# Kernel optimization log

Hardware: AMD Instinct MI355X
Metric: run time of the kernel (lower is better)

The kernel has to match this reference:

```python
import jax, jax.numpy as jnp
import numpy as np

N_, C_, D_, H_, W_ = 2, 96, 32, 64, 64
KC, VC, HEADS = 96, 96, 4


def setup_inputs() -> dict:
    key = jax.random.key(0)
    ks = jax.random.split(key, 9)
    s = 0.05
    return {
        "x": jax.random.normal(ks[0], (N_, C_, D_, H_, W_), jnp.float32),
        "Wk": jax.random.normal(ks[1], (KC, C_), jnp.float32) * s,
        "bk": jax.random.normal(ks[2], (KC,), jnp.float32) * s,
        "Wq": jax.random.normal(ks[3], (KC, C_), jnp.float32) * s,
        "bq": jax.random.normal(ks[4], (KC,), jnp.float32) * s,
        "Wv": jax.random.normal(ks[5], (VC, C_), jnp.float32) * s,
        "bv": jax.random.normal(ks[6], (VC,), jnp.float32) * s,
        "Wr": jax.random.normal(ks[7], (C_, VC), jnp.float32) * s,
        "br": jax.random.normal(ks[8], (C_,), jnp.float32) * s,
    }


def reference(x, Wk, bk, Wq, bq, Wv, bv, Wr, br):
    n, c, d, h, w = x.shape
    Nvox = d * h * w
    xf = x.reshape(n, c, Nvox)  # [n, c, N]
    # 1x1x1 convs == channel matmuls
    keys = jnp.einsum('oc,ncN->noN', Wk, xf) + bk[None, :, None]
    queries = jnp.einsum('oc,ncN->noN', Wq, xf) + bq[None, :, None]
    values = jnp.einsum('oc,ncN->noN', Wv, xf) + bv[None, :, None]
    hk = KC // HEADS
    hv = VC // HEADS
    k = keys.reshape(n, HEADS, hk, Nvox)
    q = queries.reshape(n, HEADS, hk, Nvox)
    v = values.reshape(n, HEADS, hv, Nvox)
    # key softmax over sequence (N), query softmax over head channels (hk)
    k = jax.nn.softmax(k, axis=3)
    q = jax.nn.softmax(q, axis=2)
    # context[n,h,k,v] = key @ value^T ; attended = context^T @ query
    context = jnp.einsum('nhkN,nhvN->nhkv', k, v)
    attended = jnp.einsum('nhkv,nhkN->nhvN', context, q)
    agg = attended.reshape(n, VC, Nvox)
    out = jnp.einsum('ov,nvN->noN', Wr, agg) + br[None, :, None]
    return out.reshape(n, c, d, h, w)
```

## Files before the change

kernel.cpp:

```cpp
#include <hip/hip_runtime.h>


#define NV 131072
#define CC 96
#define NB 2
#define HK 24
#define PAD 68
#define BPN 384
#define TILES_N 2048

__global__ __launch_bounds__(256) void k_prep(
    const float* __restrict__ Wq, const float* __restrict__ Wk,
    const float* __restrict__ Wv,
    float* __restrict__ Wqt, float* __restrict__ Wkt, float* __restrict__ Wvt)
{
    const int i = blockIdx.x * 256 + threadIdx.x;
    if (i >= CC * CC) return;
    const int h = i / (HK * CC);
    const int r = i % (HK * CC);
    const int c = r / HK;
    const int j = r % HK;
    const int src = (h * HK + j) * CC + c;
    Wqt[i] = Wq[src];
    Wkt[i] = Wk[src];
    Wvt[i] = Wv[src];
}

__global__ __launch_bounds__(256) void k_fused(
    const float* __restrict__ x,
    const float* __restrict__ Wqt, const float* __restrict__ bq,
    const float* __restrict__ Wkt, const float* __restrict__ bk,
    const float* __restrict__ Wvt, const float* __restrict__ bv,
    float* __restrict__ qsm, float* __restrict__ ctx, float* __restrict__ ksum)
{
    __shared__ float eks[4 * HK * PAD];
    __shared__ float vls[4 * HK * PAD];
    const int tid = threadIdx.x;
    const int pl  = tid & 63;
    const int gu  = __builtin_amdgcn_readfirstlane(tid >> 6);
    const int n   = blockIdx.x / BPN;
    const int r0  = blockIdx.x % BPN;
    const int a   = pl >> 3, b = pl & 7;

    float* __restrict__ ek = eks + gu * HK * PAD;
    float* __restrict__ vl = vls + gu * HK * PAD;
    const float* __restrict__ Wqh = Wqt + gu * HK * CC;
    const float* __restrict__ Wkh = Wkt + gu * HK * CC;
    const float* __restrict__ Wvh = Wvt + gu * HK * CC;

    float cacc[9];
#pragma unroll
    for (int k = 0; k < 9; ++k) cacc[k] = 0.f;
    float ksacc = 0.f;

    for (int tt = r0; tt < TILES_N; tt += BPN) {
        const size_t xb = (size_t)n * CC * NV + (size_t)tt * 64 + pl;

        float aq[HK], ak[HK], av[HK];
#pragma unroll
        for (int j = 0; j < HK; ++j) {
            aq[j] = bq[gu * HK + j];
            ak[j] = bk[gu * HK + j];
            av[j] = bv[gu * HK + j];
        }
        for (int ch = 0; ch < 6; ++ch) {
            float xr[16];
#pragma unroll
            for (int u = 0; u < 16; ++u)
                xr[u] = x[xb + (size_t)(ch * 16 + u) * NV];
#pragma unroll
            for (int u = 0; u < 16; ++u) {
                const float* __restrict__ w = Wqh + (ch * 16 + u) * HK;
#pragma unroll
                for (int j = 0; j < HK; ++j) aq[j] = fmaf(w[j], xr[u], aq[j]);
            }
#pragma unroll
            for (int u = 0; u < 16; ++u) {
                const float* __restrict__ w = Wkh + (ch * 16 + u) * HK;
#pragma unroll
                for (int j = 0; j < HK; ++j) ak[j] = fmaf(w[j], xr[u], ak[j]);
            }
#pragma unroll
            for (int u = 0; u < 16; ++u) {
                const float* __restrict__ w = Wvh + (ch * 16 + u) * HK;
#pragma unroll
                for (int j = 0; j < HK; ++j) av[j] = fmaf(w[j], xr[u], av[j]);
            }
        }

        {
            float mx = aq[0];
#pragma unroll
            for (int j = 1; j < HK; ++j) mx = fmaxf(mx, aq[j]);
            float s = 0.f;
#pragma unroll
            for (int j = 0; j < HK; ++j) { aq[j] = __expf(aq[j] - mx); s += aq[j]; }
            const float inv = 1.f / s;
            float4* __restrict__ qs4 = (float4*)qsm;
            const size_t qb4 = ((size_t)n * 24 + gu * 6) * NV + (size_t)tt * 64 + pl;
#pragma unroll
            for (int jj = 0; jj < 6; ++jj) {
                float4 t;
                t.x = aq[4 * jj + 0] * inv;
                t.y = aq[4 * jj + 1] * inv;
                t.z = aq[4 * jj + 2] * inv;
                t.w = aq[4 * jj + 3] * inv;
                qs4[qb4 + (size_t)jj * NV] = t;
            }
        }

#pragma unroll
        for (int j = 0; j < HK; ++j) ek[j * PAD + pl] = __expf(ak[j]);
#pragma unroll
        for (int j = 0; j < HK; ++j) vl[j * PAD + pl] = av[j];

        if (pl < HK) {
            const float4* __restrict__ rp = (const float4*)(ek + pl * PAD);
            float s = 0.f;
#pragma unroll
            for (int q = 0; q < 16; ++q) {
                const float4 t = rp[q];
                s += t.x + t.y + t.z + t.w;
            }
            ksacc += s;
        }

#pragma unroll
        for (int q = 0; q < 16; ++q) {
            float4 e4[3], v4[3];
#pragma unroll
            for (int i = 0; i < 3; ++i)
                e4[i] = ((const float4*)(ek + (a + 8 * i) * PAD))[q];
#pragma unroll
            for (int j = 0; j < 3; ++j)
                v4[j] = ((const float4*)(vl + (b + 8 * j) * PAD))[q];
#pragma unroll
            for (int i = 0; i < 3; ++i)
#pragma unroll
                for (int j = 0; j < 3; ++j) {
                    float t = cacc[i * 3 + j];
                    t = fmaf(e4[i].x, v4[j].x, t);
                    t = fmaf(e4[i].y, v4[j].y, t);
                    t = fmaf(e4[i].z, v4[j].z, t);
                    t = fmaf(e4[i].w, v4[j].w, t);
                    cacc[i * 3 + j] = t;
                }
        }
    }

#pragma unroll
    for (int i = 0; i < 3; ++i)
#pragma unroll
        for (int j = 0; j < 3; ++j)
            atomicAdd(&ctx[((size_t)n * CC + gu * HK + a + 8 * i) * HK + b + 8 * j],
                      cacc[i * 3 + j]);
    if (pl < HK) atomicAdd(&ksum[n * CC + gu * HK + pl], ksacc);
}

__global__ __launch_bounds__(256) void k_combine(
    const float* __restrict__ Wr, const float* __restrict__ ctx,
    const float* __restrict__ ksum, float* __restrict__ Mnt)
{
    const int n = blockIdx.x;
    for (int i = threadIdx.x; i < CC * CC; i += 256) {
        const int kg = i / CC, o = i % CC, h = kg / HK;
        float a = 0.f;
        for (int v = 0; v < HK; ++v)
            a += Wr[o * CC + h * HK + v] * ctx[((size_t)n * CC + kg) * HK + v];
        Mnt[((size_t)n * CC + kg) * CC + o] = a / ksum[n * CC + kg];
    }
}

__global__ __launch_bounds__(256) void k_out(
    const float* __restrict__ qsm, const float* __restrict__ Mnt,
    const float* __restrict__ br, float* __restrict__ out)
{
    const int tid = threadIdx.x;
    const int pl  = tid & 63;
    const int w   = __builtin_amdgcn_readfirstlane(tid >> 6);
    const int n   = blockIdx.x >> 10;
    const int pt  = blockIdx.x & 1023;
    const size_t p0 = (size_t)pt * 128 + pl;

    const float* __restrict__ Mb = Mnt + ((size_t)n * CC) * CC + w * HK;
    const float4* __restrict__ q4 = (const float4*)qsm + (size_t)n * 24 * NV + p0;

    float a0[HK], a1[HK];
#pragma unroll
    for (int j = 0; j < HK; ++j) { a0[j] = br[w * HK + j]; a1[j] = a0[j]; }

#pragma unroll 2
    for (int qg = 0; qg < 24; ++qg) {
        const float4 v0 = q4[(size_t)qg * NV];
        const float4 v1 = q4[(size_t)qg * NV + 64];
        const float* __restrict__ m0 = Mb + (size_t)(4 * qg + 0) * CC;
        const float* __restrict__ m1 = Mb + (size_t)(4 * qg + 1) * CC;
        const float* __restrict__ m2 = Mb + (size_t)(4 * qg + 2) * CC;
        const float* __restrict__ m3 = Mb + (size_t)(4 * qg + 3) * CC;
#pragma unroll
        for (int j = 0; j < HK; ++j) {
            a0[j] = fmaf(m0[j], v0.x, a0[j]);
            a1[j] = fmaf(m0[j], v1.x, a1[j]);
        }
#pragma unroll
        for (int j = 0; j < HK; ++j) {
            a0[j] = fmaf(m1[j], v0.y, a0[j]);
            a1[j] = fmaf(m1[j], v1.y, a1[j]);
        }
#pragma unroll
        for (int j = 0; j < HK; ++j) {
            a0[j] = fmaf(m2[j], v0.z, a0[j]);
            a1[j] = fmaf(m2[j], v1.z, a1[j]);
        }
#pragma unroll
        for (int j = 0; j < HK; ++j) {
            a0[j] = fmaf(m3[j], v0.w, a0[j]);
            a1[j] = fmaf(m3[j], v1.w, a1[j]);
        }
    }

    float* __restrict__ ob = out + ((size_t)n * CC + (size_t)w * HK) * NV + p0;
#pragma unroll
    for (int j = 0; j < HK; ++j) {
        ob[(size_t)j * NV]      = a0[j];
        ob[(size_t)j * NV + 64] = a1[j];
    }
}

extern "C" void kernel_launch(void* const* d_in, const int* in_sizes, int n_in,
                              void* d_out, int out_size, void* d_ws, size_t ws_size,
                              hipStream_t stream) {
    const float* x  = (const float*)d_in[0];
    const float* Wk = (const float*)d_in[1];
    const float* bk = (const float*)d_in[2];
    const float* Wq = (const float*)d_in[3];
    const float* bq = (const float*)d_in[4];
    const float* Wv = (const float*)d_in[5];
    const float* bv = (const float*)d_in[6];
    const float* Wr = (const float*)d_in[7];
    const float* br = (const float*)d_in[8];
    float* out = (float*)d_out;

    float* ws = (float*)d_ws;
    const size_t BIG = (size_t)NB * CC * NV;
    float* qsm  = ws;
    float* ctx  = ws + BIG;
    float* ksum = ctx + (size_t)NB * CC * HK;
    float* Mnt  = ksum + (size_t)NB * CC;
    float* Wqt  = Mnt + (size_t)NB * CC * CC;
    float* Wkt  = Wqt + CC * CC;
    float* Wvt  = Wkt + CC * CC;

    hipMemsetAsync(ctx, 0, ((size_t)NB * CC * HK + (size_t)NB * CC) * sizeof(float), stream);

    k_prep<<<dim3((CC * CC + 255) / 256), dim3(256), 0, stream>>>(Wq, Wk, Wv, Wqt, Wkt, Wvt);
    k_fused<<<dim3(NB * BPN), dim3(256), 0, stream>>>(x, Wqt, bq, Wkt, bk, Wvt, bv, qsm, ctx, ksum);
    k_combine<<<dim3(NB), dim3(256), 0, stream>>>(Wr, ctx, ksum, Mnt);
    k_out<<<dim3(NB * 1024), dim3(256), 0, stream>>>(qsm, Mnt, br, out);
}
```

Baseline: 631.8 us.

## Software-pipeline x and q loads, spread combine over many blocks

In the fused projection kernel, x channel chunks are now double-buffered: the next 16-channel chunk, and the first chunk of the next tile, are loaded while the current chunk's FMAs run. Launch bounds are raised to target 3 waves per SIMD. The q loads in the output kernel are prefetched one group ahead, and the combine kernel now uses one thread per output element across many blocks instead of 2 blocks. The aim is to hide global-load latency and the cost of a near-serial combine, at the price of higher register pressure and possible spills.

```diff
diff --git a/kernel.cpp b/kernel.cpp
--- a/kernel.cpp
+++ b/kernel.cpp
@@ -26,7 +26,7 @@
     Wvt[i] = Wv[src];
 }
 
-__global__ __launch_bounds__(256) void k_fused(
+__global__ __launch_bounds__(256, 3) void k_fused(
     const float* __restrict__ x,
     const float* __restrict__ Wqt, const float* __restrict__ bq,
     const float* __restrict__ Wkt, const float* __restrict__ bk,
@@ -53,40 +53,49 @@
     for (int k = 0; k < 9; ++k) cacc[k] = 0.f;
     float ksacc = 0.f;
 
+    float aq[HK], ak[HK], av[HK];
+    float xra[16], xrb[16];
+
+    auto CONS = [&](const float (&xr)[16], int cb) {
+#pragma unroll
+        for (int u = 0; u < 16; ++u) {
+            const int c = cb + u;
+            const float xv = xr[u];
+#pragma unroll
+            for (int j = 0; j < HK; ++j) {
+                aq[j] = fmaf(Wqh[c * HK + j], xv, aq[j]);
+                ak[j] = fmaf(Wkh[c * HK + j], xv, ak[j]);
+                av[j] = fmaf(Wvh[c * HK + j], xv, av[j]);
+            }
+        }
+    };
+    auto LD = [&](float (&xr)[16], size_t base, int cb) {
+#pragma unroll
+        for (int u = 0; u < 16; ++u)
+            xr[u] = x[base + (size_t)(cb + u) * NV];
+    };
+
+    size_t xb = (size_t)n * CC * NV + (size_t)r0 * 64 + pl;
+    LD(xra, xb, 0);
+
     for (int tt = r0; tt < TILES_N; tt += BPN) {
-        const size_t xb = (size_t)n * CC * NV + (size_t)tt * 64 + pl;
-
-        float aq[HK], ak[HK], av[HK];
+        const size_t xnext = (size_t)n * CC * NV + (size_t)(tt + BPN) * 64 + pl;
+
 #pragma unroll
         for (int j = 0; j < HK; ++j) {
             aq[j] = bq[gu * HK + j];
             ak[j] = bk[gu * HK + j];
             av[j] = bv[gu * HK + j];
         }
-        for (int ch = 0; ch < 6; ++ch) {
-            float xr[16];
-#pragma unroll
-            for (int u = 0; u < 16; ++u)
-                xr[u] = x[xb + (size_t)(ch * 16 + u) * NV];
-#pragma unroll
-            for (int u = 0; u < 16; ++u) {
-                const float* __restrict__ w = Wqh + (ch * 16 + u) * HK;
-#pragma unroll
-                for (int j = 0; j < HK; ++j) aq[j] = fmaf(w[j], xr[u], aq[j]);
-            }
-#pragma unroll
-            for (int u = 0; u < 16; ++u) {
-                const float* __restrict__ w = Wkh + (ch * 16 + u) * HK;
-#pragma unroll
-                for (int j = 0; j < HK; ++j) ak[j] = fmaf(w[j], xr[u], ak[j]);
-            }
-#pragma unroll
-            for (int u = 0; u < 16; ++u) {
-                const float* __restrict__ w = Wvh + (ch * 16 + u) * HK;
-#pragma unroll
-                for (int j = 0; j < HK; ++j) av[j] = fmaf(w[j], xr[u], av[j]);
-            }
-        }
+
+        LD(xrb, xb, 16);  CONS(xra, 0);
+        LD(xra, xb, 32);  CONS(xrb, 16);
+        LD(xrb, xb, 48);  CONS(xra, 32);
+        LD(xra, xb, 64);  CONS(xrb, 48);
+        LD(xrb, xb, 80);  CONS(xra, 64);
+        if (tt + BPN < TILES_N) LD(xra, xnext, 0);
+        CONS(xrb, 80);
+        xb = xnext;
 
         {
             float mx = aq[0];
@@ -161,14 +170,17 @@
     const float* __restrict__ Wr, const float* __restrict__ ctx,
     const float* __restrict__ ksum, float* __restrict__ Mnt)
 {
-    const int n = blockIdx.x;
-    for (int i = threadIdx.x; i < CC * CC; i += 256) {
-        const int kg = i / CC, o = i % CC, h = kg / HK;
-        float a = 0.f;
-        for (int v = 0; v < HK; ++v)
-            a += Wr[o * CC + h * HK + v] * ctx[((size_t)n * CC + kg) * HK + v];
-        Mnt[((size_t)n * CC + kg) * CC + o] = a / ksum[n * CC + kg];
-    }
+    const int g  = blockIdx.x * 256 + threadIdx.x;
+    const int n  = g / (CC * CC);
+    const int r  = g % (CC * CC);
+    const int kg = r / CC;
+    const int o  = r % CC;
+    const int h  = kg / HK;
+    float a = 0.f;
+#pragma unroll
+    for (int v = 0; v < HK; ++v)
+        a += Wr[o * CC + h * HK + v] * ctx[((size_t)n * CC + kg) * HK + v];
+    Mnt[((size_t)n * CC + kg) * CC + o] = a / ksum[n * CC + kg];
 }
 
 __global__ __launch_bounds__(256) void k_out(
@@ -189,10 +201,7 @@
 #pragma unroll
     for (int j = 0; j < HK; ++j) { a0[j] = br[w * HK + j]; a1[j] = a0[j]; }
 
-#pragma unroll 2
-    for (int qg = 0; qg < 24; ++qg) {
-        const float4 v0 = q4[(size_t)qg * NV];
-        const float4 v1 = q4[(size_t)qg * NV + 64];
+    auto FMAB = [&](int qg, const float4& v0, const float4& v1) {
         const float* __restrict__ m0 = Mb + (size_t)(4 * qg + 0) * CC;
         const float* __restrict__ m1 = Mb + (size_t)(4 * qg + 1) * CC;
         const float* __restrict__ m2 = Mb + (size_t)(4 * qg + 2) * CC;
@@ -217,7 +226,18 @@
             a0[j] = fmaf(m3[j], v0.w, a0[j]);
             a1[j] = fmaf(m3[j], v1.w, a1[j]);
         }
+    };
+
+    float4 c0 = q4[0];
+    float4 c1 = q4[64];
+#pragma unroll 4
+    for (int qg = 0; qg < 23; ++qg) {
+        const float4 n0 = q4[(size_t)(qg + 1) * NV];
+        const float4 n1 = q4[(size_t)(qg + 1) * NV + 64];
+        FMAB(qg, c0, c1);
+        c0 = n0; c1 = n1;
     }
+    FMAB(23, c0, c1);
 
     float* __restrict__ ob = out + ((size_t)n * CC + (size_t)w * HK) * NV + p0;
 #pragma unroll
@@ -255,6 +275,6 @@
 
     k_prep<<<dim3((CC * CC + 255) / 256), dim3(256), 0, stream>>>(Wq, Wk, Wv, Wqt, Wkt, Wvt);
     k_fused<<<dim3(NB * BPN), dim3(256), 0, stream>>>(x, Wqt, bq, Wkt, bk, Wvt, bv, qsm, ctx, ksum);
-    k_combine<<<dim3(NB), dim3(256), 0, stream>>>(Wr, ctx, ksum, Mnt);
+    k_combine<<<dim3(NB * CC * CC / 256), dim3(256), 0, stream>>>(Wr, ctx, ksum, Mnt);
     k_out<<<dim3(NB * 1024), dim3(256), 0, stream>>>(qsm, Mnt, br, out);
 }
```

New measurement: 891.3 us. +41.1%, slower.
